# Optimization experiments

Measured on AMD Instinct MI355X. Metric: run time of the kernel, lower is better.

## Reference

```python
import jax, jax.numpy as jnp
import numpy as np

EPS = 1e-6

def _ste(x, xq):
    return x + jax.lax.stop_gradient(xq - x)

def rmsnorm(x, w):
    return x * jax.lax.rsqrt(jnp.mean(x * x, axis=-1, keepdims=True) + EPS) * w

def act_quant(x):
    # per-token absmax int8 quantization (BitNet b1.58)
    s = 127.0 / jnp.clip(jnp.max(jnp.abs(x), axis=-1, keepdims=True), 1e-5)
    return _ste(x, jnp.clip(jnp.round(x * s), -128, 127) / s)

def w_quant(w):
    # per-tensor mean-absmax ternary quantization
    s = 1.0 / jnp.clip(jnp.mean(jnp.abs(w)), 1e-5)
    return _ste(w, jnp.clip(jnp.round(w * s), -1, 1) / s)

def bitlinear(x, w):
    return act_quant(x) @ w_quant(w).T

def snake_beta(x, log_a, log_b):
    a = jnp.exp(log_a)
    b = jnp.exp(log_b)
    s = jnp.sin(a * x)
    return x + (1.0 / (b + 1e-9)) * s * s

def ffn(x, nw, w1, la, lb, w2):
    h = bitlinear(rmsnorm(x, nw), w1)
    return bitlinear(snake_beta(h, la, lb), w2)

def mha(x, nw, ipw, ipb, opw, opb, num_heads):
    B, T, D = x.shape
    hd = D // num_heads
    xn = rmsnorm(x, nw)
    qkv = xn @ ipw.T + ipb  # [B,T,3D]
    q, k, v = jnp.split(qkv, 3, axis=-1)
    def heads(t):
        return t.reshape(B, T, num_heads, hd).transpose(0, 2, 1, 3)  # [B,H,T,hd]
    q, k, v = heads(q), heads(k), heads(v)
    scores = jnp.einsum('bhqd,bhkd->bhqk', q, k) / jnp.sqrt(jnp.asarray(hd, x.dtype))
    attn = jax.nn.softmax(scores, axis=-1)
    o = jnp.einsum('bhqk,bhkd->bhqd', attn, v)
    o = o.transpose(0, 2, 1, 3).reshape(B, T, D)
    return o @ opw.T + opb

def conv_branch(x, nw, pw1, dw, dwb, bg, bb, bm, bv, la, lb, pw2, K):
    B, T, D = x.shape
    h = rmsnorm(x, nw)
    h = bitlinear(h, pw1)  # [B,T,2D] (1x1 BitConv1d)
    a, g = jnp.split(h, 2, axis=-1)
    h = a * jax.nn.sigmoid(g)  # GLU over channels
    hc = h.transpose(0, 2, 1)  # [B,D,T]
    hc = jax.lax.conv_general_dilated(
        hc, dw, window_strides=(1,), padding=[(K // 2, K // 2)],
        feature_group_count=D, dimension_numbers=('NCH', 'OIH', 'NCH'))
    hc = hc + dwb[None, :, None]
    hc = (hc - bm[None, :, None]) * jax.lax.rsqrt(bv[None, :, None] + 1e-5) * bg[None, :, None] + bb[None, :, None]
    h = hc.transpose(0, 2, 1)  # [B,T,D]
    h = snake_beta(h, la, lb)
    return bitlinear(h, pw2)

def setup_inputs() -> dict:
    key = jax.random.key(0)
    B, T, D, H, K = 4, 2048, 512, 8, 31
    ks = jax.random.split(key, 16)
    n = lambda k, s: (jax.random.normal(k, s, jnp.float32) * 0.02)
    d = {
        'x': jax.random.normal(ks[0], (B, T, D), jnp.float32),
        'ff1_norm_w': jnp.ones((D,), jnp.float32),
        'ff1_w1': n(ks[1], (4 * D, D)), 'ff1_a': jnp.zeros((4 * D,), jnp.float32),
        'ff1_b': jnp.zeros((4 * D,), jnp.float32), 'ff1_w2': n(ks[2], (D, 4 * D)),
        'attn_norm_w': jnp.ones((D,), jnp.float32),
        'in_proj_w': n(ks[3], (3 * D, D)), 'in_proj_b': jnp.zeros((3 * D,), jnp.float32),
        'out_proj_w': n(ks[4], (D, D)), 'out_proj_b': jnp.zeros((D,), jnp.float32),
        'conv_norm_w': jnp.ones((D,), jnp.float32),
        'pw1_w': n(ks[5], (2 * D, D)),
        'dw_w': n(ks[6], (D, 1, K)), 'dw_b': jnp.zeros((D,), jnp.float32),
        'bn_g': jnp.ones((D,), jnp.float32), 'bn_b': jnp.zeros((D,), jnp.float32),
        'bn_m': jnp.zeros((D,), jnp.float32), 'bn_v': jnp.ones((D,), jnp.float32),
        'snake_a': jnp.zeros((D,), jnp.float32), 'snake_b': jnp.zeros((D,), jnp.float32),
        'pw2_w': n(ks[7], (D, D)),
        'ff2_norm_w': jnp.ones((D,), jnp.float32),
        'ff2_w1': n(ks[8], (4 * D, D)), 'ff2_a': jnp.zeros((4 * D,), jnp.float32),
        'ff2_b': jnp.zeros((4 * D,), jnp.float32), 'ff2_w2': n(ks[9], (D, 4 * D)),
        'final_norm_w': jnp.ones((D,), jnp.float32),
    }
    return d

def reference(x, ff1_norm_w, ff1_w1, ff1_a, ff1_b, ff1_w2, attn_norm_w, in_proj_w, in_proj_b, out_proj_w, out_proj_b, conv_norm_w, pw1_w, dw_w, dw_b, bn_g, bn_b, bn_m, bn_v, snake_a, snake_b, pw2_w, ff2_norm_w, ff2_w1, ff2_a, ff2_b, ff2_w2, final_norm_w):
    H, K = 8, 31
    x = x + 0.5 * ffn(x, ff1_norm_w, ff1_w1, ff1_a, ff1_b, ff1_w2)
    x = x + mha(x, attn_norm_w, in_proj_w, in_proj_b, out_proj_w, out_proj_b, H)
    x = x + conv_branch(x, conv_norm_w, pw1_w, dw_w, dw_b, bn_g, bn_b, bn_m, bn_v, snake_a, snake_b, pw2_w, K)
    x = x + 0.5 * ffn(x, ff2_norm_w, ff2_w1, ff2_a, ff2_b, ff2_w2)
    return rmsnorm(x, final_norm_w)
```

## Files before the change

### kernel.cpp

```cpp
#include <hip/hip_runtime.h>
#include <math.h>


typedef int   v4i __attribute__((ext_vector_type(4)));
typedef float v4f __attribute__((ext_vector_type(4)));
typedef float v16f __attribute__((ext_vector_type(16)));
typedef short v8s __attribute__((ext_vector_type(8)));
typedef unsigned short u16;

#define GLOAD_LDS(g, l) __builtin_amdgcn_global_load_lds( \
    (const __attribute__((address_space(1))) void*)(g),   \
    (__attribute__((address_space(3))) void*)(l), 16, 0, 0)

__device__ __forceinline__ float blk_sum256(float v, float* sm) {
#pragma unroll
  for (int m = 32; m; m >>= 1) v += __shfl_xor(v, m);
  int w = threadIdx.x >> 6;
  __syncthreads();
  if ((threadIdx.x & 63) == 0) sm[w] = v;
  __syncthreads();
  return sm[0] + sm[1] + sm[2] + sm[3];
}

__device__ __forceinline__ float blk_max256(float v, float* sm) {
#pragma unroll
  for (int m = 32; m; m >>= 1) v = fmaxf(v, __shfl_xor(v, m));
  int w = threadIdx.x >> 6;
  __syncthreads();
  if ((threadIdx.x & 63) == 0) sm[w] = v;
  __syncthreads();
  return fmaxf(fmaxf(sm[0], sm[1]), fmaxf(sm[2], sm[3]));
}

__device__ __forceinline__ u16 f2bf(float f) {
  union { float f; unsigned u; } x;
  x.f = f;
  unsigned r = x.u + 0x7fffu + ((x.u >> 16) & 1u);
  return (u16)(r >> 16);
}

__device__ __forceinline__ float bf2f(u16 u) {
  union { unsigned u; float f; } x;
  x.u = ((unsigned)u) << 16;
  return x.f;
}

__device__ __forceinline__ void xcd_tiles(int BNlog_unused, int& tx, int& ty) {
  int nx = gridDim.x;
  int flat = blockIdx.y * nx + blockIdx.x;
  int nwg = nx * gridDim.y;
  int cpx = nwg >> 3;
  int swz = (flat & 7) * cpx + (flat >> 3);
  ty = swz / nx;
  tx = swz - ty * nx;
}

__global__ __launch_bounds__(256) void wabs_stage1(
    const float* __restrict__ w0, const float* __restrict__ w1,
    const float* __restrict__ w2, const float* __restrict__ w3,
    const float* __restrict__ w4, const float* __restrict__ w5,
    float* __restrict__ part) {
  __shared__ float sm[4];
  const float* ws[6] = {w0, w1, w2, w3, w4, w5};
  const int ns[6] = {1048576, 1048576, 524288, 262144, 1048576, 1048576};
  int widx = blockIdx.x >> 6;
  int chunk = blockIdx.x & 63;
  const float* w = ws[widx];
  int n = ns[widx];
  float s = 0.f;
  for (int i = chunk * 256 + threadIdx.x; i < n; i += 64 * 256) s += fabsf(w[i]);
  s = blk_sum256(s, sm);
  if (threadIdx.x == 0) part[widx * 64 + chunk] = s;
}

__global__ __launch_bounds__(256) void wquant_all(
    const float* __restrict__ w0, const float* __restrict__ w1,
    const float* __restrict__ w2, const float* __restrict__ w3,
    const float* __restrict__ w4, const float* __restrict__ w5,
    const float* __restrict__ part, float* __restrict__ scales,
    signed char* __restrict__ out) {
  const float* ws[6] = {w0, w1, w2, w3, w4, w5};
  const int ns[6] = {1048576, 1048576, 524288, 262144, 1048576, 1048576};
  const int offs[6] = {0, 1048576, 2097152, 2621440, 2883584, 3932160};
  int widx = blockIdx.y;
  const float* w = ws[widx];
  int n = ns[widx];
  signed char* o = out + offs[widx];
  float ssum = 0.f;
#pragma unroll 8
  for (int i = 0; i < 64; ++i) ssum += part[widx * 64 + i];
  float wsc = fmaxf(ssum / (float)n, 1e-5f);
  if (blockIdx.x == 0 && threadIdx.x == 0) scales[widx] = wsc;
  float s = 1.0f / wsc;
  for (int i = blockIdx.x * 256 + threadIdx.x; i < n; i += 128 * 256)
    o[i] = (signed char)(int)fminf(fmaxf(rintf(w[i] * s), -1.f), 1.f);
}

__global__ __launch_bounds__(256) void wcvt_tabs(
    const float* __restrict__ ip, const float* __restrict__ op, u16* __restrict__ wb,
    const float* __restrict__ a1, const float* __restrict__ b1,
    const float* __restrict__ a2, const float* __restrict__ b2,
    float* __restrict__ tabs) {
  int bid = blockIdx.x;
  if (bid < 4096) {
    int i = bid * 256 + threadIdx.x;
    if (i < 786432) wb[i] = f2bf(ip[i]);
    else wb[i] = f2bf(op[i - 786432]);
  } else {
    int i = (bid - 4096) * 256 + threadIdx.x;
    if (i < 2048) {
      tabs[i] = __expf(a1[i]);
      tabs[2048 + i] = 1.0f / (__expf(b1[i]) + 1e-9f);
      tabs[4096 + i] = __expf(a2[i]);
      tabs[6144 + i] = 1.0f / (__expf(b2[i]) + 1e-9f);
    }
  }
}

__global__ __launch_bounds__(256) void rmsnorm_multi(
    const float* __restrict__ x, const float* __restrict__ w, int mode,
    float* __restrict__ outf, signed char* __restrict__ out8,
    u16* __restrict__ outb, float* __restrict__ dq) {
  __shared__ float sm[4];
  int row = blockIdx.x, tid = threadIdx.x;
  const float* xr = x + (size_t)row * 512;
  float v0 = xr[tid], v1 = xr[tid + 256];
  float ss = blk_sum256(v0 * v0 + v1 * v1, sm);
  float sc = 1.0f / sqrtf(ss * (1.0f / 512.0f) + 1e-6f);
  float y0 = v0 * sc * w[tid];
  float y1 = v1 * sc * w[tid + 256];
  size_t o = (size_t)row * 512 + tid;
  if (mode == 0) {
    outf[o] = y0; outf[o + 256] = y1;
  } else if (mode == 1) {
    float am = blk_max256(fmaxf(fabsf(y0), fabsf(y1)), sm);
    float amc = fmaxf(am, 1e-5f);
    float s = 127.0f / amc;
    out8[o] = (signed char)(int)rintf(y0 * s);
    out8[o + 256] = (signed char)(int)rintf(y1 * s);
    if (tid == 0) dq[row] = amc * (1.0f / 127.0f);
  } else {
    outb[o] = f2bf(y0); outb[o + 256] = f2bf(y1);
  }
}

__global__ __launch_bounds__(256) void snake_q8(
    const u16* __restrict__ h, const float* __restrict__ ta, const float* __restrict__ tb,
    signed char* __restrict__ out, float* __restrict__ dq) {
  __shared__ float sm[4];
  int row = blockIdx.x, tid = threadIdx.x;
  const u16* hr = h + (size_t)row * 2048;
  int c0 = tid * 8;
  v8s hv = *(const v8s*)(hr + c0);
  float4 ta0 = *(const float4*)(ta + c0);
  float4 ta1 = *(const float4*)(ta + c0 + 4);
  float4 tb0 = *(const float4*)(tb + c0);
  float4 tb1 = *(const float4*)(tb + c0 + 4);
  float sa[8] = {ta0.x, ta0.y, ta0.z, ta0.w, ta1.x, ta1.y, ta1.z, ta1.w};
  float sib[8] = {tb0.x, tb0.y, tb0.z, tb0.w, tb1.x, tb1.y, tb1.z, tb1.w};
  float vals[8];
  float am = 0.f;
#pragma unroll
  for (int j = 0; j < 8; ++j) {
    float v = bf2f((u16)hv[j]);
    float s = __sinf(sa[j] * v);
    v += s * s * sib[j];
    vals[j] = v;
    am = fmaxf(am, fabsf(v));
  }
  am = blk_max256(am, sm);
  float amc = fmaxf(am, 1e-5f);
  float s = 127.0f / amc;
  unsigned long long pkt = 0;
#pragma unroll
  for (int j = 0; j < 8; ++j) {
    int q = (int)rintf(vals[j] * s);
    pkt |= ((unsigned long long)(unsigned char)(signed char)q) << (8 * j);
  }
  *(unsigned long long*)(out + (size_t)row * 2048 + c0) = pkt;
  if (tid == 0) dq[row] = amc * (1.0f / 127.0f);
}

__global__ __launch_bounds__(256) void rowquant512_bf(
    const u16* __restrict__ in, signed char* __restrict__ out, float* __restrict__ dq) {
  __shared__ float sm[4];
  int row = blockIdx.x, tid = threadIdx.x;
  unsigned pv = *(const unsigned*)(in + (size_t)row * 512 + tid * 2);
  float v0 = bf2f((u16)pv), v1 = bf2f((u16)(pv >> 16));
  float am = blk_max256(fmaxf(fabsf(v0), fabsf(v1)), sm);
  float amc = fmaxf(am, 1e-5f);
  float s = 127.0f / amc;
  signed char q0 = (signed char)(int)rintf(v0 * s);
  signed char q1 = (signed char)(int)rintf(v1 * s);
  unsigned short pk = (unsigned short)((unsigned char)q0 | ((unsigned)(unsigned char)q1 << 8));
  *(unsigned short*)(out + (size_t)row * 512 + tid * 2) = pk;
  if (tid == 0) dq[row] = amc * (1.0f / 127.0f);
}

template <int BN, bool OBF>
__global__ __launch_bounds__(256) void gemm_i8_t(
    const signed char* __restrict__ A, const signed char* __restrict__ B,
    const float* __restrict__ wsp, const float* __restrict__ adq,
    const float* __restrict__ resid, float rscale,
    float* __restrict__ outf, u16* __restrict__ outb, int N, int K) {
  constexpr int JF = BN / 32;
  __shared__ signed char As[16384];
  __shared__ signed char Bs[BN * 128];
  const int tid = threadIdx.x;
  int txc, tyc;
  xcd_tiles(0, txc, tyc);
  const int m0 = tyc << 7;
  const int n0 = txc * BN;
  const int lane = tid & 63;
  const int wv = tid >> 6;
  const int wr = (wv >> 1) << 6, wc = (wv & 1) * (16 * JF);
  const int r15 = lane & 15, khi = lane >> 4;
  const int srow = tid >> 3;
  const int sslot = (tid & 7) ^ (srow & 7);
  const signed char* Ag = A + (size_t)(m0 + srow) * K + sslot * 16;
  const signed char* Bg = B + (size_t)(n0 + srow) * K + sslot * 16;
  const size_t row32 = (size_t)32 * K;

  int aoff[4][2], boff[JF][2];
#pragma unroll
  for (int i = 0; i < 4; ++i) {
    int r = wr + i * 16 + r15;
#pragma unroll
    for (int s = 0; s < 2; ++s)
      aoff[i][s] = r * 128 + (((s << 2) + khi) ^ (r & 7)) * 16;
  }
#pragma unroll
  for (int j = 0; j < JF; ++j) {
    int c = wc + j * 16 + r15;
#pragma unroll
    for (int s = 0; s < 2; ++s)
      boff[j][s] = c * 128 + (((s << 2) + khi) ^ (c & 7)) * 16;
  }
  v4i acc[4][JF] = {};
  for (int k0 = 0; k0 < K; k0 += 128) {
    __syncthreads();
#pragma unroll
    for (int c = 0; c < 4; ++c)
      GLOAD_LDS(Ag + c * row32 + k0, As + c * 4096 + tid * 16);
#pragma unroll
    for (int c = 0; c < BN / 32; ++c)
      GLOAD_LDS(Bg + c * row32 + k0, Bs + c * 4096 + tid * 16);
    __syncthreads();
    v4i a[4][2], b[JF][2];
#pragma unroll
    for (int i = 0; i < 4; ++i) {
      a[i][0] = *(const v4i*)(As + aoff[i][0]);
      a[i][1] = *(const v4i*)(As + aoff[i][1]);
    }
#pragma unroll
    for (int j = 0; j < JF; ++j) {
      b[j][0] = *(const v4i*)(Bs + boff[j][0]);
      b[j][1] = *(const v4i*)(Bs + boff[j][1]);
    }
#pragma unroll
    for (int i = 0; i < 4; ++i)
#pragma unroll
      for (int j = 0; j < JF; ++j) {
        acc[i][j] = __builtin_amdgcn_mfma_i32_16x16x64_i8(a[i][0], b[j][0], acc[i][j], 0, 0, 0);
        acc[i][j] = __builtin_amdgcn_mfma_i32_16x16x64_i8(a[i][1], b[j][1], acc[i][j], 0, 0, 0);
      }
  }
  const float wsc = *wsp;
#pragma unroll
  for (int i = 0; i < 4; ++i) {
    int rb = m0 + wr + i * 16 + (khi << 2);
    float dqv[4];
#pragma unroll
    for (int rr = 0; rr < 4; ++rr) dqv[rr] = adq[rb + rr] * wsc;
#pragma unroll
    for (int j = 0; j < JF; ++j) {
      int col = n0 + wc + j * 16 + r15;
#pragma unroll
      for (int rr = 0; rr < 4; ++rr) {
        size_t idx = (size_t)(rb + rr) * N + col;
        float v = (float)acc[i][j][rr] * dqv[rr];
        if constexpr (OBF) outb[idx] = f2bf(v);
        else outf[idx] = resid ? fmaf(rscale, v, resid[idx]) : v;
      }
    }
  }
}

template <int BN, bool OBF>
__global__ __launch_bounds__(256) void gemm_bf16_t(
    const u16* __restrict__ A, const u16* __restrict__ B,
    const float* __restrict__ bias, const float* __restrict__ resid,
    float* __restrict__ outf, u16* __restrict__ outb, int N, int K) {
  constexpr int JF = BN / 32;
  __shared__ signed char As[8192];
  __shared__ signed char Bs[BN * 64];
  const int tid = threadIdx.x;
  int txc, tyc;
  xcd_tiles(0, txc, tyc);
  const int m0 = tyc << 7;
  const int n0 = txc * BN;
  const int lane = tid & 63;
  const int wv = tid >> 6;
  const int wr = (wv >> 1) << 6, wc = (wv & 1) * (16 * JF);
  const int r15 = lane & 15, khi = lane >> 4;
  const int srow = tid >> 2;
  const int sslot = (tid & 3) ^ ((srow >> 1) & 3);
  const int K2 = K * 2;
  const signed char* Ag = (const signed char*)A + (size_t)(m0 + srow) * K2 + sslot * 16;
  const signed char* Bg = (const signed char*)B + (size_t)(n0 + srow) * K2 + sslot * 16;
  const size_t half = (size_t)64 * K2;

  int aoff[4], boff[JF];
#pragma unroll
  for (int i = 0; i < 4; ++i) {
    int r = wr + i * 16 + r15;
    aoff[i] = r * 64 + ((khi ^ ((r >> 1) & 3)) << 4);
  }
#pragma unroll
  for (int j = 0; j < JF; ++j) {
    int c = wc + j * 16 + r15;
    boff[j] = c * 64 + ((khi ^ ((c >> 1) & 3)) << 4);
  }
  v4f acc[4][JF] = {};
  for (int kb = 0; kb < K2; kb += 64) {
    __syncthreads();
    GLOAD_LDS(Ag + kb, As + tid * 16);
    GLOAD_LDS(Ag + half + kb, As + 4096 + tid * 16);
    GLOAD_LDS(Bg + kb, Bs + tid * 16);
    if constexpr (BN == 128) GLOAD_LDS(Bg + half + kb, Bs + 4096 + tid * 16);
    __syncthreads();
    v8s a[4], b[JF];
#pragma unroll
    for (int i = 0; i < 4; ++i) a[i] = *(const v8s*)(As + aoff[i]);
#pragma unroll
    for (int j = 0; j < JF; ++j) b[j] = *(const v8s*)(Bs + boff[j]);
#pragma unroll
    for (int i = 0; i < 4; ++i)
#pragma unroll
      for (int j = 0; j < JF; ++j)
        acc[i][j] = __builtin_amdgcn_mfma_f32_16x16x32_bf16(a[i], b[j], acc[i][j], 0, 0, 0);
  }
#pragma unroll
  for (int i = 0; i < 4; ++i) {
    int rb = m0 + wr + i * 16 + (khi << 2);
#pragma unroll
    for (int j = 0; j < JF; ++j) {
      int col = n0 + wc + j * 16 + r15;
      float bv = bias[col];
#pragma unroll
      for (int rr = 0; rr < 4; ++rr) {
        size_t idx = (size_t)(rb + rr) * N + col;
        float v = acc[i][j][rr] + bv;
        if constexpr (OBF) outb[idx] = f2bf(v);
        else outf[idx] = resid[idx] + v;
      }
    }
  }
}

__global__ __launch_bounds__(256) void kvqpack(
    const u16* __restrict__ qkv, u16* __restrict__ kvqp) {
  __shared__ u16 Lv[32 * 72];
  const int tid = threadIdx.x;
  const int tile = blockIdx.x;
  const int bh = blockIdx.y;
  const int b = bh >> 3, h = bh & 7;
  u16* outb = kvqp + ((size_t)(bh * 64 + tile)) * 6144;
  const int lane = tid & 63, f = tid >> 6;
  const int l31 = lane & 31, hi = lane >> 5;

  {
    int r = tid >> 3, c = (tid & 7) << 3;
    const u16* src = qkv + (size_t)(b * 2048 + tile * 32 + r) * 1536 + 1024 + h * 64 + c;
    *(v8s*)(&Lv[r * 72 + c]) = *(const v8s*)src;
  }
  {
    const u16* src = qkv + (size_t)(b * 2048 + tile * 32 + l31) * 1536 + h * 64 + f * 16 + hi * 8;
    *(v8s*)(outb + (size_t)(8 + f) * 512 + lane * 8) = *(const v8s*)src;
  }
  {
    const u16* src = qkv + (size_t)(b * 2048 + tile * 32 + l31) * 1536 + 512 + h * 64 + f * 16 + hi * 8;
    *(v8s*)(outb + (size_t)f * 512 + lane * 8) = *(const v8s*)src;
  }
  __syncthreads();
  {
    int d = ((f >> 1) << 5) + l31;
    int tbase = ((f & 1) << 4) + hi * 8;
    v8s v;
#pragma unroll
    for (int j = 0; j < 8; ++j) v[j] = (short)Lv[(tbase + j) * 72 + d];
    *(v8s*)(outb + (size_t)(4 + f) * 512 + lane * 8) = v;
  }
}

__global__ __launch_bounds__(256) void attn32(
    const u16* __restrict__ kvqp, u16* __restrict__ opart, float* __restrict__ ml) {
  __shared__ u16 KV[2][4096];
  const int tid = threadIdx.x;
  const int lane = tid & 63;
  const int wv = tid >> 6;
  const int l31 = lane & 31;
  const int hi = lane >> 5;
  const int bh = blockIdx.y;
  const int z = blockIdx.z;
  const int b = bh >> 3, h = bh & 7;
  const int qt = blockIdx.x * 4 + wv;
  const int q0 = qt << 5;
  const float C = 0.18033688011112042f;

  v8s qf[4];
  {
    const u16* qb = kvqp + ((size_t)(bh * 64 + qt)) * 6144 + lane * 8;
#pragma unroll
    for (int ks = 0; ks < 4; ++ks) qf[ks] = *(const v8s*)(qb + (8 + ks) * 512);
  }
  v16f o0 = {}, o1 = {};
  float m_run = -INFINITY, l_run = 0.f;

  const u16* tb = kvqp + ((size_t)(bh * 64 + z * 16)) * 6144;

  GLOAD_LDS(tb + tid * 8, &KV[0][tid * 8]);
  GLOAD_LDS(tb + 2048 + tid * 8, &KV[0][2048 + tid * 8]);
  __syncthreads();

  int cur = 0;
  for (int t = 0; t < 16; ++t) {
    if (t < 15) {
      const u16* nb = tb + (size_t)(t + 1) * 6144;
      GLOAD_LDS(nb + tid * 8, &KV[cur ^ 1][tid * 8]);
      GLOAD_LDS(nb + 2048 + tid * 8, &KV[cur ^ 1][2048 + tid * 8]);
    }
    v8s kf[4], vf[4];
#pragma unroll
    for (int ks = 0; ks < 4; ++ks) kf[ks] = *(const v8s*)(&KV[cur][ks * 512 + lane * 8]);
#pragma unroll
    for (int j = 0; j < 4; ++j) vf[j] = *(const v8s*)(&KV[cur][2048 + j * 512 + lane * 8]);

    __builtin_amdgcn_s_setprio(1);
    v16f sacc = {};
#pragma unroll
    for (int ks = 0; ks < 4; ++ks)
      sacc = __builtin_amdgcn_mfma_f32_32x32x16_bf16(kf[ks], qf[ks], sacc, 0, 0, 0);
    __builtin_amdgcn_s_setprio(0);

    float s[16];
#pragma unroll
    for (int r = 0; r < 16; ++r) s[r] = sacc[r];
    float m0v = fmaxf(fmaxf(s[0], s[1]), s[2]);
    float m1v = fmaxf(fmaxf(s[3], s[4]), s[5]);
    float m2v = fmaxf(fmaxf(s[6], s[7]), s[8]);
    float m3v = fmaxf(fmaxf(s[9], s[10]), s[11]);
    float m4v = fmaxf(fmaxf(s[12], s[13]), s[14]);
    float t0v = fmaxf(fmaxf(m0v, m1v), m2v);
    float t1v = fmaxf(fmaxf(m3v, m4v), s[15]);
    float mx = fmaxf(t0v, t1v);
    {
      float tsw = mx;
      asm("v_permlane32_swap_b32 %0, %1" : "+v"(tsw), "+v"(mx));
      mx = fmaxf(mx, tsw);
    }
    if (__any((mx - m_run) * C > 8.0f)) {
      float mn = fmaxf(m_run, mx);
      float corr = exp2f((m_run - mn) * C);
      m_run = mn;
      l_run *= corr;
#pragma unroll
      for (int r = 0; r < 16; ++r) { o0[r] *= corr; o1[r] *= corr; }
    }
    float mnC = m_run * C;
#pragma unroll
    for (int r = 0; r < 16; ++r) s[r] = exp2f(fmaf(s[r], C, -mnC));

    {
      float a0 = (s[0] + s[1]) + (s[2] + s[3]);
      float a1 = (s[4] + s[5]) + (s[6] + s[7]);
      float a2 = (s[8] + s[9]) + (s[10] + s[11]);
      float a3 = (s[12] + s[13]) + (s[14] + s[15]);
      float ls = (a0 + a1) + (a2 + a3);
      float tsw = ls;
      asm("v_permlane32_swap_b32 %0, %1" : "+v"(tsw), "+v"(ls));
      l_run += ls + tsw;
    }

    unsigned pk[8];
#pragma unroll
    for (int g = 0; g < 8; ++g) {
      unsigned u;
      asm("v_cvt_pk_bf16_f32 %0, %1, %2" : "=v"(u) : "v"(s[2 * g]), "v"(s[2 * g + 1]));
      pk[g] = u;
    }
    asm("v_permlane32_swap_b32 %0, %1" : "+v"(pk[2]), "+v"(pk[0]));
    asm("v_permlane32_swap_b32 %0, %1" : "+v"(pk[3]), "+v"(pk[1]));
    asm("v_permlane32_swap_b32 %0, %1" : "+v"(pk[6]), "+v"(pk[4]));
    asm("v_permlane32_swap_b32 %0, %1" : "+v"(pk[7]), "+v"(pk[5]));
    v4i w0, w1;
    w0[0] = pk[0]; w0[1] = pk[1]; w0[2] = pk[2]; w0[3] = pk[3];
    w1[0] = pk[4]; w1[1] = pk[5]; w1[2] = pk[6]; w1[3] = pk[7];
    v8s pf0 = *(v8s*)&w0;
    v8s pf1 = *(v8s*)&w1;

    __builtin_amdgcn_s_setprio(1);
    o0 = __builtin_amdgcn_mfma_f32_32x32x16_bf16(vf[0], pf0, o0, 0, 0, 0);
    o0 = __builtin_amdgcn_mfma_f32_32x32x16_bf16(vf[1], pf1, o0, 0, 0, 0);
    o1 = __builtin_amdgcn_mfma_f32_32x32x16_bf16(vf[2], pf0, o1, 0, 0, 0);
    o1 = __builtin_amdgcn_mfma_f32_32x32x16_bf16(vf[3], pf1, o1, 0, 0, 0);
    __builtin_amdgcn_s_setprio(0);

    __syncthreads();
    cur ^= 1;
  }

  float inv = 1.0f / l_run;
  u16* orow = opart + (size_t)z * 4194304 + (size_t)(b * 2048 + q0 + l31) * 512 + h * 64;
#pragma unroll
  for (int dt = 0; dt < 2; ++dt) {
#pragma unroll
    for (int g = 0; g < 8; ++g) {
      int d = dt * 32 + ((2 * g) & 3) + 8 * (g >> 1) + 4 * hi;
      float a = (dt ? o1[2 * g] : o0[2 * g]) * inv;
      float bv = (dt ? o1[2 * g + 1] : o0[2 * g + 1]) * inv;
      unsigned u;
      asm("v_cvt_pk_bf16_f32 %0, %1, %2" : "=v"(u) : "v"(a), "v"(bv));
      *(unsigned*)(orow + d) = u;
    }
  }
  if (hi == 0) {
    size_t mi = ((size_t)(z * 8192 + b * 2048 + q0 + l31) * 8 + h) * 2;
    ml[mi] = m_run;
    ml[mi + 1] = l_run;
  }
}

__global__ __launch_bounds__(256) void attn_merge(
    const u16* __restrict__ opart, const float* __restrict__ ml,
    u16* __restrict__ attno) {
  __shared__ float wsm[4][8];
  const int r = blockIdx.x, tid = threadIdx.x;
  if (tid < 8) {
    const float C = 0.18033688011112042f;
    float m[4], l[4];
#pragma unroll
    for (int z = 0; z < 4; ++z) {
      size_t i = ((size_t)(z * 8192 + r) * 8 + tid) * 2;
      m[z] = ml[i];
      l[z] = ml[i + 1];
    }
    float M = fmaxf(fmaxf(m[0], m[1]), fmaxf(m[2], m[3]));
    float a[4], sum = 0.f;
#pragma unroll
    for (int z = 0; z < 4; ++z) {
      a[z] = exp2f((m[z] - M) * C) * l[z];
      sum += a[z];
    }
    float inv = 1.0f / sum;
#pragma unroll
    for (int z = 0; z < 4; ++z) wsm[z][tid] = a[z] * inv;
  }
  __syncthreads();
  int c = tid * 2;
  int hh = c >> 6;
  float x0 = 0.f, x1 = 0.f;
#pragma unroll
  for (int z = 0; z < 4; ++z) {
    unsigned p = *(const unsigned*)(opart + (size_t)z * 4194304 + (size_t)r * 512 + c);
    float w = wsm[z][hh];
    x0 = fmaf(bf2f((u16)p), w, x0);
    x1 = fmaf(bf2f((u16)(p >> 16)), w, x1);
  }
  unsigned u;
  asm("v_cvt_pk_bf16_f32 %0, %1, %2" : "=v"(u) : "v"(x0), "v"(x1));
  *(unsigned*)(attno + (size_t)r * 512 + c) = u;
}

__global__ __launch_bounds__(256) void dwconv_fused(
    const u16* __restrict__ g3, const float* __restrict__ dww,
    const float* __restrict__ dwb, const float* __restrict__ bng,
    const float* __restrict__ bnb, const float* __restrict__ bnm,
    const float* __restrict__ bnv, const float* __restrict__ la,
    const float* __restrict__ lb, u16* __restrict__ outp) {
  __shared__ float IN[160 * 64];
  __shared__ float WT[1984];
  __shared__ float PRM[4][64];
  const int tid = threadIdx.x;
  const int cg = blockIdx.x << 6;
  const int t0 = blockIdx.y << 7;
  const int bb = blockIdx.z;

  if (tid < 64) {
    int c = cg + tid;
    float sc = bng[c] / sqrtf(bnv[c] + 1e-5f);
    PRM[0][tid] = sc;
    PRM[1][tid] = (dwb[c] - bnm[c]) * sc + bnb[c];
    PRM[2][tid] = __expf(la[c]);
    PRM[3][tid] = 1.0f / (__expf(lb[c]) + 1e-9f);
  }
  for (int i = tid; i < 1984; i += 256) WT[i] = dww[cg * 31 + i];

#pragma unroll
  for (int p = 0; p < 5; ++p) {
    int r = p * 32 + (tid >> 3);
    int t = t0 - 16 + r;
    int c8 = (tid & 7) << 3;
    float4 lo = make_float4(0.f, 0.f, 0.f, 0.f);
    float4 hv = make_float4(0.f, 0.f, 0.f, 0.f);
    if (t >= 0 && t < 2048) {
      const u16* rp = g3 + ((size_t)(bb * 2048 + t)) * 1024 + cg + c8;
      v8s a8 = *(const v8s*)rp;
      v8s g8 = *(const v8s*)(rp + 512);
      float va[8];
#pragma unroll
      for (int j = 0; j < 8; ++j) {
        float fa = bf2f((u16)a8[j]);
        float fg = bf2f((u16)g8[j]);
        va[j] = fa / (1.f + __expf(-fg));
      }
      lo = make_float4(va[0], va[1], va[2], va[3]);
      hv = make_float4(va[4], va[5], va[6], va[7]);
    }
    *(float4*)&IN[r * 64 + c8] = lo;
    *(float4*)&IN[r * 64 + c8 + 4] = hv;
  }
  __syncthreads();

  const int ch = tid & 63;
  const int tg = tid >> 6;
  const float sc = PRM[0][ch], sh = PRM[1][ch], sa = PRM[2][ch], sib = PRM[3][ch];
  float w[31];
#pragma unroll
  for (int k = 0; k < 31; ++k) w[k] = WT[ch * 31 + k];

  for (int pass = 0; pass < 4; ++pass) {
    int tl = pass * 32 + tg * 8;
    float x[38];
#pragma unroll
    for (int i = 0; i < 38; ++i) x[i] = IN[(tl + 1 + i) * 64 + ch];
    float acc[8] = {0.f, 0.f, 0.f, 0.f, 0.f, 0.f, 0.f, 0.f};
#pragma unroll
    for (int k = 0; k < 31; ++k)
#pragma unroll
      for (int j = 0; j < 8; ++j) acc[j] = fmaf(x[k + j], w[k], acc[j]);
#pragma unroll
    for (int j = 0; j < 8; ++j) {
      float v = acc[j] * sc + sh;
      float s = __sinf(sa * v);
      v += s * s * sib;
      outp[((size_t)(bb * 2048 + t0 + tl + j)) * 512 + cg + ch] = f2bf(v);
    }
  }
}

extern "C" void kernel_launch(void* const* d_in, const int* in_sizes, int n_in,
                              void* d_out, int out_size, void* d_ws, size_t ws_size,
                              hipStream_t stream) {
  const float* x_in = (const float*)d_in[0];
  const float* ff1_norm_w = (const float*)d_in[1];
  const float* ff1_w1 = (const float*)d_in[2];
  const float* ff1_a = (const float*)d_in[3];
  const float* ff1_b = (const float*)d_in[4];
  const float* ff1_w2 = (const float*)d_in[5];
  const float* attn_norm_w = (const float*)d_in[6];
  const float* in_proj_w = (const float*)d_in[7];
  const float* in_proj_b = (const float*)d_in[8];
  const float* out_proj_w = (const float*)d_in[9];
  const float* out_proj_b = (const float*)d_in[10];
  const float* conv_norm_w = (const float*)d_in[11];
  const float* pw1_w = (const float*)d_in[12];
  const float* dw_w = (const float*)d_in[13];
  const float* dw_b = (const float*)d_in[14];
  const float* bn_g = (const float*)d_in[15];
  const float* bn_b = (const float*)d_in[16];
  const float* bn_m = (const float*)d_in[17];
  const float* bn_v = (const float*)d_in[18];
  const float* snake_a = (const float*)d_in[19];
  const float* snake_b = (const float*)d_in[20];
  const float* pw2_w = (const float*)d_in[21];
  const float* ff2_norm_w = (const float*)d_in[22];
  const float* ff2_w1 = (const float*)d_in[23];
  const float* ff2_a = (const float*)d_in[24];
  const float* ff2_b = (const float*)d_in[25];
  const float* ff2_w2 = (const float*)d_in[26];
  const float* final_norm_w = (const float*)d_in[27];
  float* out = (float*)d_out;

  char* ws = (char*)d_ws;
  float* x_cur = (float*)(ws + 0);
  u16* qkv = (u16*)(ws + 16777216);
  u16* kvqp = (u16*)(ws + 41943040);
  u16* opart = (u16*)(ws + 67108864);
  u16* attno = (u16*)(ws + 100663296);
  float* ml = (float*)(ws + 109051904);
  u16* h_b = (u16*)(ws + 16777216);
  u16* g3b = (u16*)(ws + 16777216);
  u16* convout = (u16*)(ws + 50331648);
  signed char* a8a = (signed char*)(ws + 83886080);
  signed char* a8b = (signed char*)(ws + 88080384);
  u16* xnb = (u16*)(ws + 104857600);
  signed char* wq = (signed char*)(ws + 113246208);
  signed char* wq_w1 = wq;
  signed char* wq_w2 = wq + 1048576;
  signed char* wq_p1 = wq + 2097152;
  signed char* wq_p2 = wq + 2621440;
  signed char* wq_f21 = wq + 2883584;
  signed char* wq_f22 = wq + 3932160;
  u16* wb = (u16*)(ws + 118226944);
  u16* wb_ip = wb;
  u16* wb_op = wb + 786432;
  float* scales = (float*)(ws + 120324096);
  float* partials = (float*)(ws + 120324352);
  float* ascale = (float*)(ws + 120325888);
  float* tabs = (float*)(ws + 120358912);

  wabs_stage1<<<384, 256, 0, stream>>>(ff1_w1, ff1_w2, pw1_w, pw2_w, ff2_w1, ff2_w2, partials);
  wquant_all<<<dim3(128, 6), 256, 0, stream>>>(ff1_w1, ff1_w2, pw1_w, pw2_w, ff2_w1, ff2_w2,
                                               partials, scales, wq);
  wcvt_tabs<<<4104, 256, 0, stream>>>(in_proj_w, out_proj_w, wb, ff1_a, ff1_b, ff2_a, ff2_b,
                                      tabs);

  rmsnorm_multi<<<8192, 256, 0, stream>>>(x_in, ff1_norm_w, 1, nullptr, a8a, nullptr, ascale);
  gemm_i8_t<128, true><<<dim3(16, 64), 256, 0, stream>>>(
      a8a, wq_w1, scales + 0, ascale, nullptr, 1.0f, nullptr, h_b, 2048, 512);
  snake_q8<<<8192, 256, 0, stream>>>(h_b, tabs, tabs + 2048, a8b, ascale);
  gemm_i8_t<64, false><<<dim3(8, 64), 256, 0, stream>>>(
      a8b, wq_w2, scales + 1, ascale, x_in, 0.5f, x_cur, nullptr, 512, 2048);

  rmsnorm_multi<<<8192, 256, 0, stream>>>(x_cur, attn_norm_w, 2, nullptr, nullptr, xnb, nullptr);
  gemm_bf16_t<128, true><<<dim3(12, 64), 256, 0, stream>>>(
      xnb, wb_ip, in_proj_b, nullptr, nullptr, qkv, 1536, 512);
  kvqpack<<<dim3(64, 32), 256, 0, stream>>>(qkv, kvqp);
  attn32<<<dim3(16, 32, 4), 256, 0, stream>>>(kvqp, opart, ml);
  attn_merge<<<8192, 256, 0, stream>>>(opart, ml, attno);
  gemm_bf16_t<64, false><<<dim3(8, 64), 256, 0, stream>>>(
      attno, wb_op, out_proj_b, x_cur, x_cur, nullptr, 512, 512);

  rmsnorm_multi<<<8192, 256, 0, stream>>>(x_cur, conv_norm_w, 1, nullptr, a8a, nullptr, ascale);
  gemm_i8_t<128, true><<<dim3(8, 64), 256, 0, stream>>>(
      a8a, wq_p1, scales + 2, ascale, nullptr, 1.0f, nullptr, g3b, 1024, 512);
  dwconv_fused<<<dim3(8, 16, 4), 256, 0, stream>>>(g3b, dw_w, dw_b, bn_g, bn_b, bn_m, bn_v,
                                                   snake_a, snake_b, convout);
  rowquant512_bf<<<8192, 256, 0, stream>>>(convout, a8a, ascale);
  gemm_i8_t<64, false><<<dim3(8, 64), 256, 0, stream>>>(
      a8a, wq_p2, scales + 3, ascale, x_cur, 1.0f, x_cur, nullptr, 512, 512);

  rmsnorm_multi<<<8192, 256, 0, stream>>>(x_cur, ff2_norm_w, 1, nullptr, a8a, nullptr, ascale);
  gemm_i8_t<128, true><<<dim3(16, 64), 256, 0, stream>>>(
      a8a, wq_f21, scales + 4, ascale, nullptr, 1.0f, nullptr, h_b, 2048, 512);
  snake_q8<<<8192, 256, 0, stream>>>(h_b, tabs + 4096, tabs + 6144, a8b, ascale);
  gemm_i8_t<64, false><<<dim3(8, 64), 256, 0, stream>>>(
      a8b, wq_f22, scales + 5, ascale, x_cur, 0.5f, x_cur, nullptr, 512, 2048);

  rmsnorm_multi<<<8192, 256, 0, stream>>>(x_cur, final_norm_w, 0, out, nullptr, nullptr, nullptr);
}
```

Measured before the change: 348.2 us.

## Store residual stream in bf16 and use one-wave-per-row norm kernels

The fp32 residual stream x_cur becomes a bf16 buffer. The input is converted to bf16 inside the setup kernel, and the GEMM epilogues read and write the residual as bf16. The row-norm and row-quant kernels are rewritten so each wave handles one 512-wide row with vectorized 8-element loads and pure shuffle reductions, launching 4x fewer blocks with no LDS barriers. This cuts residual memory traffic, but rounding the residual to bf16 at every sublayer adds accumulated error that may hurt accuracy against the fp32 reference.

```diff
diff --git a/kernel.cpp b/kernel.cpp
--- a/kernel.cpp
+++ b/kernel.cpp
@@ -45,7 +45,7 @@
   return x.f;
 }
 
-__device__ __forceinline__ void xcd_tiles(int BNlog_unused, int& tx, int& ty) {
+__device__ __forceinline__ void xcd_tiles(int& tx, int& ty) {
   int nx = gridDim.x;
   int flat = blockIdx.y * nx + blockIdx.x;
   int nwg = nx * gridDim.y;
@@ -100,13 +100,13 @@
     const float* __restrict__ ip, const float* __restrict__ op, u16* __restrict__ wb,
     const float* __restrict__ a1, const float* __restrict__ b1,
     const float* __restrict__ a2, const float* __restrict__ b2,
-    float* __restrict__ tabs) {
+    float* __restrict__ tabs, const float* __restrict__ x, u16* __restrict__ xbf) {
   int bid = blockIdx.x;
   if (bid < 4096) {
     int i = bid * 256 + threadIdx.x;
     if (i < 786432) wb[i] = f2bf(ip[i]);
     else wb[i] = f2bf(op[i - 786432]);
-  } else {
+  } else if (bid < 4104) {
     int i = (bid - 4096) * 256 + threadIdx.x;
     if (i < 2048) {
       tabs[i] = __expf(a1[i]);
@@ -114,33 +114,69 @@
       tabs[4096 + i] = __expf(a2[i]);
       tabs[6144 + i] = 1.0f / (__expf(b2[i]) + 1e-9f);
     }
-  }
-}
-
-__global__ __launch_bounds__(256) void rmsnorm_multi(
-    const float* __restrict__ x, const float* __restrict__ w, int mode,
+  } else {
+    size_t i = ((size_t)(bid - 4104) * 256 + threadIdx.x) * 8;
+    float4 f0 = *(const float4*)(x + i);
+    float4 f1 = *(const float4*)(x + i + 4);
+    v8s o;
+    o[0] = (short)f2bf(f0.x); o[1] = (short)f2bf(f0.y);
+    o[2] = (short)f2bf(f0.z); o[3] = (short)f2bf(f0.w);
+    o[4] = (short)f2bf(f1.x); o[5] = (short)f2bf(f1.y);
+    o[6] = (short)f2bf(f1.z); o[7] = (short)f2bf(f1.w);
+    *(v8s*)(xbf + i) = o;
+  }
+}
+
+__global__ __launch_bounds__(256) void rmsnorm_wave(
+    const u16* __restrict__ x, const float* __restrict__ w, int mode,
     float* __restrict__ outf, signed char* __restrict__ out8,
     u16* __restrict__ outb, float* __restrict__ dq) {
-  __shared__ float sm[4];
-  int row = blockIdx.x, tid = threadIdx.x;
-  const float* xr = x + (size_t)row * 512;
-  float v0 = xr[tid], v1 = xr[tid + 256];
-  float ss = blk_sum256(v0 * v0 + v1 * v1, sm);
+  const int tid = threadIdx.x;
+  const int lane = tid & 63, wv = tid >> 6;
+  const int row = blockIdx.x * 4 + wv;
+  const int c0 = lane * 8;
+  v8s xv = *(const v8s*)(x + (size_t)row * 512 + c0);
+  float v[8];
+  float ss = 0.f;
+#pragma unroll
+  for (int j = 0; j < 8; ++j) {
+    v[j] = bf2f((u16)xv[j]);
+    ss = fmaf(v[j], v[j], ss);
+  }
+#pragma unroll
+  for (int m = 1; m < 64; m <<= 1) ss += __shfl_xor(ss, m);
   float sc = 1.0f / sqrtf(ss * (1.0f / 512.0f) + 1e-6f);
-  float y0 = v0 * sc * w[tid];
-  float y1 = v1 * sc * w[tid + 256];
-  size_t o = (size_t)row * 512 + tid;
+  float4 w0 = *(const float4*)(w + c0);
+  float4 w1 = *(const float4*)(w + c0 + 4);
+  float wv8[8] = {w0.x, w0.y, w0.z, w0.w, w1.x, w1.y, w1.z, w1.w};
+  float y[8];
+#pragma unroll
+  for (int j = 0; j < 8; ++j) y[j] = v[j] * sc * wv8[j];
   if (mode == 0) {
-    outf[o] = y0; outf[o + 256] = y1;
+    float* o = outf + (size_t)row * 512 + c0;
+    *(float4*)o = make_float4(y[0], y[1], y[2], y[3]);
+    *(float4*)(o + 4) = make_float4(y[4], y[5], y[6], y[7]);
   } else if (mode == 1) {
-    float am = blk_max256(fmaxf(fabsf(y0), fabsf(y1)), sm);
+    float am = 0.f;
+#pragma unroll
+    for (int j = 0; j < 8; ++j) am = fmaxf(am, fabsf(y[j]));
+#pragma unroll
+    for (int m = 1; m < 64; m <<= 1) am = fmaxf(am, __shfl_xor(am, m));
     float amc = fmaxf(am, 1e-5f);
     float s = 127.0f / amc;
-    out8[o] = (signed char)(int)rintf(y0 * s);
-    out8[o + 256] = (signed char)(int)rintf(y1 * s);
-    if (tid == 0) dq[row] = amc * (1.0f / 127.0f);
+    unsigned long long pkt = 0;
+#pragma unroll
+    for (int j = 0; j < 8; ++j) {
+      int q = (int)rintf(y[j] * s);
+      pkt |= ((unsigned long long)(unsigned char)(signed char)q) << (8 * j);
+    }
+    *(unsigned long long*)(out8 + (size_t)row * 512 + c0) = pkt;
+    if (lane == 0) dq[row] = amc * (1.0f / 127.0f);
   } else {
-    outb[o] = f2bf(y0); outb[o + 256] = f2bf(y1);
+    v8s o;
+#pragma unroll
+    for (int j = 0; j < 8; ++j) o[j] = (short)f2bf(y[j]);
+    *(v8s*)(outb + (size_t)row * 512 + c0) = o;
   }
 }
 
@@ -181,34 +217,46 @@
   if (tid == 0) dq[row] = amc * (1.0f / 127.0f);
 }
 
-__global__ __launch_bounds__(256) void rowquant512_bf(
+__global__ __launch_bounds__(256) void rowquant_wave(
     const u16* __restrict__ in, signed char* __restrict__ out, float* __restrict__ dq) {
-  __shared__ float sm[4];
-  int row = blockIdx.x, tid = threadIdx.x;
-  unsigned pv = *(const unsigned*)(in + (size_t)row * 512 + tid * 2);
-  float v0 = bf2f((u16)pv), v1 = bf2f((u16)(pv >> 16));
-  float am = blk_max256(fmaxf(fabsf(v0), fabsf(v1)), sm);
+  const int tid = threadIdx.x;
+  const int lane = tid & 63, wv = tid >> 6;
+  const int row = blockIdx.x * 4 + wv;
+  const int c0 = lane * 8;
+  v8s xv = *(const v8s*)(in + (size_t)row * 512 + c0);
+  float v[8];
+  float am = 0.f;
+#pragma unroll
+  for (int j = 0; j < 8; ++j) {
+    v[j] = bf2f((u16)xv[j]);
+    am = fmaxf(am, fabsf(v[j]));
+  }
+#pragma unroll
+  for (int m = 1; m < 64; m <<= 1) am = fmaxf(am, __shfl_xor(am, m));
   float amc = fmaxf(am, 1e-5f);
   float s = 127.0f / amc;
-  signed char q0 = (signed char)(int)rintf(v0 * s);
-  signed char q1 = (signed char)(int)rintf(v1 * s);
-  unsigned short pk = (unsigned short)((unsigned char)q0 | ((unsigned)(unsigned char)q1 << 8));
-  *(unsigned short*)(out + (size_t)row * 512 + tid * 2) = pk;
-  if (tid == 0) dq[row] = amc * (1.0f / 127.0f);
-}
-
-template <int BN, bool OBF>
+  unsigned long long pkt = 0;
+#pragma unroll
+  for (int j = 0; j < 8; ++j) {
+    int q = (int)rintf(v[j] * s);
+    pkt |= ((unsigned long long)(unsigned char)(signed char)q) << (8 * j);
+  }
+  *(unsigned long long*)(out + (size_t)row * 512 + c0) = pkt;
+  if (lane == 0) dq[row] = amc * (1.0f / 127.0f);
+}
+
+template <int BN, int OM>
 __global__ __launch_bounds__(256) void gemm_i8_t(
     const signed char* __restrict__ A, const signed char* __restrict__ B,
     const float* __restrict__ wsp, const float* __restrict__ adq,
-    const float* __restrict__ resid, float rscale,
-    float* __restrict__ outf, u16* __restrict__ outb, int N, int K) {
+    const u16* __restrict__ resid, float rscale,
+    u16* __restrict__ outb, int N, int K) {
   constexpr int JF = BN / 32;
   __shared__ signed char As[16384];
   __shared__ signed char Bs[BN * 128];
   const int tid = threadIdx.x;
   int txc, tyc;
-  xcd_tiles(0, txc, tyc);
+  xcd_tiles(txc, tyc);
   const int m0 = tyc << 7;
   const int n0 = txc * BN;
   const int lane = tid & 63;
@@ -279,24 +327,24 @@
       for (int rr = 0; rr < 4; ++rr) {
         size_t idx = (size_t)(rb + rr) * N + col;
         float v = (float)acc[i][j][rr] * dqv[rr];
-        if constexpr (OBF) outb[idx] = f2bf(v);
-        else outf[idx] = resid ? fmaf(rscale, v, resid[idx]) : v;
+        if constexpr (OM == 0) outb[idx] = f2bf(v);
+        else outb[idx] = f2bf(fmaf(rscale, v, bf2f(resid[idx])));
       }
     }
   }
 }
 
-template <int BN, bool OBF>
+template <int BN, int OM>
 __global__ __launch_bounds__(256) void gemm_bf16_t(
     const u16* __restrict__ A, const u16* __restrict__ B,
-    const float* __restrict__ bias, const float* __restrict__ resid,
-    float* __restrict__ outf, u16* __restrict__ outb, int N, int K) {
+    const float* __restrict__ bias, const u16* __restrict__ resid,
+    u16* __restrict__ outb, int N, int K) {
   constexpr int JF = BN / 32;
   __shared__ signed char As[8192];
   __shared__ signed char Bs[BN * 64];
   const int tid = threadIdx.x;
   int txc, tyc;
-  xcd_tiles(0, txc, tyc);
+  xcd_tiles(txc, tyc);
   const int m0 = tyc << 7;
   const int n0 = txc * BN;
   const int lane = tid & 63;
@@ -351,8 +399,8 @@
       for (int rr = 0; rr < 4; ++rr) {
         size_t idx = (size_t)(rb + rr) * N + col;
         float v = acc[i][j][rr] + bv;
-        if constexpr (OBF) outb[idx] = f2bf(v);
-        else outf[idx] = resid[idx] + v;
+        if constexpr (OM == 0) outb[idx] = f2bf(v);
+        else outb[idx] = f2bf(bf2f(resid[idx]) + v);
       }
     }
   }
@@ -683,7 +731,8 @@
   float* out = (float*)d_out;
 
   char* ws = (char*)d_ws;
-  float* x_cur = (float*)(ws + 0);
+  u16* x_bf = (u16*)(ws + 0);
+  u16* x_cur = (u16*)(ws + 8388608);
   u16* qkv = (u16*)(ws + 16777216);
   u16* kvqp = (u16*)(ws + 41943040);
   u16* opart = (u16*)(ws + 67108864);
@@ -713,40 +762,40 @@
   wabs_stage1<<<384, 256, 0, stream>>>(ff1_w1, ff1_w2, pw1_w, pw2_w, ff2_w1, ff2_w2, partials);
   wquant_all<<<dim3(128, 6), 256, 0, stream>>>(ff1_w1, ff1_w2, pw1_w, pw2_w, ff2_w1, ff2_w2,
                                                partials, scales, wq);
-  wcvt_tabs<<<4104, 256, 0, stream>>>(in_proj_w, out_proj_w, wb, ff1_a, ff1_b, ff2_a, ff2_b,
-                                      tabs);
-
-  rmsnorm_multi<<<8192, 256, 0, stream>>>(x_in, ff1_norm_w, 1, nullptr, a8a, nullptr, ascale);
-  gemm_i8_t<128, true><<<dim3(16, 64), 256, 0, stream>>>(
-      a8a, wq_w1, scales + 0, ascale, nullptr, 1.0f, nullptr, h_b, 2048, 512);
+  wcvt_tabs<<<6152, 256, 0, stream>>>(in_proj_w, out_proj_w, wb, ff1_a, ff1_b, ff2_a, ff2_b,
+                                      tabs, x_in, x_bf);
+
+  rmsnorm_wave<<<2048, 256, 0, stream>>>(x_bf, ff1_norm_w, 1, nullptr, a8a, nullptr, ascale);
+  gemm_i8_t<128, 0><<<dim3(16, 64), 256, 0, stream>>>(
+      a8a, wq_w1, scales + 0, ascale, nullptr, 1.0f, h_b, 2048, 512);
   snake_q8<<<8192, 256, 0, stream>>>(h_b, tabs, tabs + 2048, a8b, ascale);
-  gemm_i8_t<64, false><<<dim3(8, 64), 256, 0, stream>>>(
-      a8b, wq_w2, scales + 1, ascale, x_in, 0.5f, x_cur, nullptr, 512, 2048);
-
-  rmsnorm_multi<<<8192, 256, 0, stream>>>(x_cur, attn_norm_w, 2, nullptr, nullptr, xnb, nullptr);
-  gemm_bf16_t<128, true><<<dim3(12, 64), 256, 0, stream>>>(
-      xnb, wb_ip, in_proj_b, nullptr, nullptr, qkv, 1536, 512);
+  gemm_i8_t<64, 1><<<dim3(8, 64), 256, 0, stream>>>(
+      a8b, wq_w2, scales + 1, ascale, x_bf, 0.5f, x_cur, 512, 2048);
+
+  rmsnorm_wave<<<2048, 256, 0, stream>>>(x_cur, attn_norm_w, 2, nullptr, nullptr, xnb, nullptr);
+  gemm_bf16_t<128, 0><<<dim3(12, 64), 256, 0, stream>>>(
+      xnb, wb_ip, in_proj_b, nullptr, qkv, 1536, 512);
   kvqpack<<<dim3(64, 32), 256, 0, stream>>>(qkv, kvqp);
   attn32<<<dim3(16, 32, 4), 256, 0, stream>>>(kvqp, opart, ml);
   attn_merge<<<8192, 256, 0, stream>>>(opart, ml, attno);
-  gemm_bf16_t<64, false><<<dim3(8, 64), 256, 0, stream>>>(
-      attno, wb_op, out_proj_b, x_cur, x_cur, nullptr, 512, 512);
-
-  rmsnorm_multi<<<8192, 256, 0, stream>>>(x_cur, conv_norm_w, 1, nullptr, a8a, nullptr, ascale);
-  gemm_i8_t<128, true><<<dim3(8, 64), 256, 0, stream>>>(
-      a8a, wq_p1, scales + 2, ascale, nullptr, 1.0f, nullptr, g3b, 1024, 512);
+  gemm_bf16_t<64, 1><<<dim3(8, 64), 256, 0, stream>>>(
+      attno, wb_op, out_proj_b, x_cur, x_cur, 512, 512);
+
+  rmsnorm_wave<<<2048, 256, 0, stream>>>(x_cur, conv_norm_w, 1, nullptr, a8a, nullptr, ascale);
+  gemm_i8_t<128, 0><<<dim3(8, 64), 256, 0, stream>>>(
+      a8a, wq_p1, scales + 2, ascale, nullptr, 1.0f, g3b, 1024, 512);
   dwconv_fused<<<dim3(8, 16, 4), 256, 0, stream>>>(g3b, dw_w, dw_b, bn_g, bn_b, bn_m, bn_v,
                                                    snake_a, snake_b, convout);
-  rowquant512_bf<<<8192, 256, 0, stream>>>(convout, a8a, ascale);
-  gemm_i8_t<64, false><<<dim3(8, 64), 256, 0, stream>>>(
-      a8a, wq_p2, scales + 3, ascale, x_cur, 1.0f, x_cur, nullptr, 512, 512);
-
-  rmsnorm_multi<<<8192, 256, 0, stream>>>(x_cur, ff2_norm_w, 1, nullptr, a8a, nullptr, ascale);
-  gemm_i8_t<128, true><<<dim3(16, 64), 256, 0, stream>>>(
-      a8a, wq_f21, scales + 4, ascale, nullptr, 1.0f, nullptr, h_b, 2048, 512);
+  rowquant_wave<<<2048, 256, 0, stream>>>(convout, a8a, ascale);
+  gemm_i8_t<64, 1><<<dim3(8, 64), 256, 0, stream>>>(
+      a8a, wq_p2, scales + 3, ascale, x_cur, 1.0f, x_cur, 512, 512);
+
+  rmsnorm_wave<<<2048, 256, 0, stream>>>(x_cur, ff2_norm_w, 1, nullptr, a8a, nullptr, ascale);
+  gemm_i8_t<128, 0><<<dim3(16, 64), 256, 0, stream>>>(
+      a8a, wq_f21, scales + 4, ascale, nullptr, 1.0f, h_b, 2048, 512);
   snake_q8<<<8192, 256, 0, stream>>>(h_b, tabs + 4096, tabs + 6144, a8b, ascale);
-  gemm_i8_t<64, false><<<dim3(8, 64), 256, 0, stream>>>(
-      a8b, wq_f22, scales + 5, ascale, x_cur, 0.5f, x_cur, nullptr, 512, 2048);
-
-  rmsnorm_multi<<<8192, 256, 0, stream>>>(x_cur, final_norm_w, 0, out, nullptr, nullptr, nullptr);
-}
+  gemm_i8_t<64, 1><<<dim3(8, 64), 256, 0, stream>>>(
+      a8b, wq_f22, scales + 5, ascale, x_cur, 0.5f, x_cur, 512, 2048);
+
+  rmsnorm_wave<<<2048, 256, 0, stream>>>(x_cur, final_norm_w, 0, out, nullptr, nullptr, nullptr);
+}
```

Result: faster. 310.5 us (-10.9%).
